# Kernel optimization log

Hardware: AMD Instinct MI355X
Metric: run time of the kernel (lower is better)

Reference implementation:

```python
import jax, jax.numpy as jnp
import numpy as np
from jax import lax


def setup_inputs() -> dict:
    key = jax.random.key(0)
    kx, kw = jax.random.split(key)
    x = jax.random.normal(kx, (32, 3, 8192), dtype=jnp.float32)
    weight = jax.random.normal(kw, (128, 3, 64), dtype=jnp.float32)
    return {"x": x, "weight": weight}


def reference(x, weight):
    # x: [B, C, L], weight: [O, C, K]
    K = weight.shape[2]
    # Cross-correlation (conv1d, no bias, valid padding): [B, O, L-K+1]
    conv_out = lax.conv_general_dilated(
        x, weight, window_strides=(1,), padding='VALID',
        dimension_numbers=('NCH', 'OIH', 'NCH'))
    # Half squared norm of each shapelet: [O]
    w_norm = jnp.sum(weight ** 2, axis=(1, 2)) / 2
    # Half squared norm of each length-K window, via cumulative sums
    # (avoids materializing the [B, C, W, K] unfold tensor)
    sq = jnp.sum(x ** 2, axis=1)               # [B, L]
    c = jnp.pad(jnp.cumsum(sq, axis=1), ((0, 0), (1, 0)))  # [B, L+1]
    win_norm = (c[:, K:] - c[:, :-K]) / 2      # [B, L-K+1]
    # features = conv_out - (||w||^2/2 + ||window||^2/2)
    features = conv_out - w_norm[None, :, None] - win_norm[:, None, :]
    # global max-pool over time, then *(-2) -> min squared distance
    return -2.0 * jnp.max(features, axis=-1)   # [B, O]
```

## Files before the change

### kernel.cpp

```cpp
#include <hip/hip_runtime.h>
#include <float.h>

#define BB 32
#define LL 8192
#define OO 128
#define KK 64
#define WW (LL - KK + 1)
#define NCH 2
#define GX 16

typedef __attribute__((ext_vector_type(8))) short short8;
typedef __attribute__((ext_vector_type(4))) float f32x4;

union AB { int4 i4; int i[4]; short8 v; };

static __device__ __forceinline__ unsigned int f2bf(float f) {
    unsigned int u = __builtin_bit_cast(unsigned int, f);
    return (u + 0x7FFFu + ((u >> 16) & 1u)) >> 16;
}

__global__ __launch_bounds__(256) void prep_kernel(const float* __restrict__ w,
                                                   unsigned short* __restrict__ wswz,
                                                   float* __restrict__ wn) {
    int g = blockIdx.x * 256 + threadIdx.x;
    if (g < 3072) {
        int ob = (g >= 1536) ? 1 : 0;
        int gg = g - ob * 1536;
        int ksqp = gg >> 6;
        int o2   = gg & 63;
        int ks = ksqp >> 2, qp = ksqp & 3;
        int c = ks >> 1, h = ks & 1;
        const float4* p = (const float4*)(w + (ob * 64 + o2) * 192 + c * 64 + h * 32 + qp * 8);
        float4 v0 = p[0], v1 = p[1];
        int4 pk;
        pk.x = (int)(f2bf(v0.x) | (f2bf(v0.y) << 16));
        pk.y = (int)(f2bf(v0.z) | (f2bf(v0.w) << 16));
        pk.z = (int)(f2bf(v1.x) | (f2bf(v1.y) << 16));
        pk.w = (int)(f2bf(v1.z) | (f2bf(v1.w) << 16));
        ((int4*)wswz)[g] = pk;
    }
    int oo = g - 3072;
    if (oo >= 0 && oo < OO) {
        const float* p = w + oo * 192;
        float s = 0.f;
        for (int i = 0; i < 192; ++i) { float v = p[i]; s = fmaf(v, v, s); }
        wn[oo] = 0.5f * s;
    }
}

static __device__ __forceinline__ void stage_chunk(const float* __restrict__ x, int b, int T0,
                                                   unsigned short* xl, float* sql, float* Pl,
                                                   int tid) {
    if (tid < 240) {
        int c = tid / 80, j4 = tid - c * 80;
        int l = T0 + j4 * 4;
        float4 v = make_float4(0.f, 0.f, 0.f, 0.f);
        if (l < LL) v = *(const float4*)(x + (b * 3 + c) * LL + l);
        uint2 pk;
        pk.x = f2bf(v.x) | (f2bf(v.y) << 16);
        pk.y = f2bf(v.z) | (f2bf(v.w) << 16);
        *(uint2*)(xl + c * 320 + j4 * 4) = pk;
    }
    {
        int l = T0 + tid;
        float s = 0.f;
        if (l < LL) {
            #pragma unroll
            for (int c = 0; c < 3; ++c) {
                float v = x[(b * 3 + c) * LL + l];
                s = fmaf(v, v, s);
            }
        }
        sql[tid] = s;
        float s8 = s + __shfl_xor(s, 1, 64);
        s8 += __shfl_xor(s8, 2, 64);
        s8 += __shfl_xor(s8, 4, 64);
        if ((tid & 7) == 0) Pl[tid >> 3] = s8;
    }
    if (tid < 64) {
        int j = 256 + tid, l = T0 + j;
        float s = 0.f;
        if (l < LL) {
            #pragma unroll
            for (int c = 0; c < 3; ++c) {
                float v = x[(b * 3 + c) * LL + l];
                s = fmaf(v, v, s);
            }
        }
        sql[j] = s;
        float s8 = s + __shfl_xor(s, 1, 64);
        s8 += __shfl_xor(s8, 2, 64);
        s8 += __shfl_xor(s8, 4, 64);
        if ((tid & 7) == 0) Pl[32 + (tid >> 3)] = s8;
    }
}

__global__ __launch_bounds__(256, 3) void shapeconv_main(const float* __restrict__ x,
                                                         const unsigned short* __restrict__ wswz,
                                                         const float* __restrict__ wn,
                                                         float* __restrict__ partial) {
    __shared__ __align__(16) unsigned short w_lds[64 * 192];
    __shared__ __align__(16) unsigned short x_lds[2][3 * 320];
    __shared__ __align__(16) float sq_lds[2][320];
    __shared__ float P_lds[2][40];
    __shared__ float mred[64];

    const int tcx = blockIdx.x;
    const int ob = blockIdx.y;
    const int b  = blockIdx.z;
    const int tid = threadIdx.x;
    const int wv = tid >> 6;
    const int lane = tid & 63;
    const int wo = wv & 1, wt = wv >> 1;
    const int n  = lane & 15;
    const int qp = lane >> 4;
    const int Tb = tcx * (NCH * 256);

    {
        const char* src = (const char*)(wswz + ob * 1536 * 8) + tid * 16;
        #pragma unroll
        for (int i = 0; i < 6; ++i) {
            __builtin_amdgcn_global_load_lds(
                (const __attribute__((address_space(1))) unsigned int*)(src + i * 4096),
                (__attribute__((address_space(3))) unsigned int*)((char*)w_lds + wv * 1024 + i * 4096),
                16, 0, 0);
        }
    }

    float wnv[2][4];
    #pragma unroll
    for (int ot = 0; ot < 2; ++ot)
        #pragma unroll
        for (int rg = 0; rg < 4; ++rg)
            wnv[ot][rg] = wn[ob * 64 + 32 * wo + 16 * ot + 4 * qp + rg];

    stage_chunk(x, b, Tb, x_lds[0], sq_lds[0], P_lds[0], tid);

    float m2[2][4];
    #pragma unroll
    for (int ot = 0; ot < 2; ++ot)
        #pragma unroll
        for (int rg = 0; rg < 4; ++rg) m2[ot][rg] = -FLT_MAX;

    #pragma unroll
    for (int ci = 0; ci < NCH; ++ci) {
        const int bsel = ci & 1;
        const int T0 = Tb + ci * 256;
        __syncthreads();

        if (ci + 1 < NCH)
            stage_chunk(x, b, T0 + 256, x_lds[1 - bsel], sq_lds[1 - bsel], P_lds[1 - bsel], tid);

        float wlm[8];
        {
            const float* sql = sq_lds[bsel];
            const float* Pl  = P_lds[bsel];
            int a = 16 * wt + n;
            float4 H0 = *(const float4*)(sql + 8 * a);
            float4 H1 = *(const float4*)(sql + 8 * a + 4);
            float4 G0 = *(const float4*)(sql + 8 * a + 64);
            float4 G1 = *(const float4*)(sql + 8 * a + 68);
            float h[8] = {H0.x, H0.y, H0.z, H0.w, H1.x, H1.y, H1.z, H1.w};
            float g[8] = {G0.x, G0.y, G0.z, G0.w, G1.x, G1.y, G1.z, G1.w};
            float s = 0.f;
            #pragma unroll
            for (int i = 1; i <= 7; ++i) s += Pl[a + i];
            #pragma unroll
            for (int j = 0; j < 8; ++j) s += h[j];
            int tg0 = T0 + 8 * a;
            #pragma unroll
            for (int r = 0; r < 8; ++r) {
                wlm[r] = (tg0 + r < WW) ? 0.5f * s : 1e30f;
                s = s - h[r] + g[r];
            }
        }

        f32x4 acc[2][8];
        #pragma unroll
        for (int ot = 0; ot < 2; ++ot)
            #pragma unroll
            for (int rg = 0; rg < 4; ++rg)
                #pragma unroll
                for (int r = 0; r < 8; ++r)
                    acc[ot][r][rg] = -wnv[ot][rg] - wlm[r];

        const char* xb = (const char*)x_lds[bsel];
        #pragma unroll
        for (int ks = 0; ks < 6; ++ks) {
            int c = ks >> 1, h2 = ks & 1;
            int e0b = c * 640 + 256 * wt + 64 * h2 + 16 * (n + qp);
            int4 Ea = *(const int4*)(xb + e0b);
            int4 Eb = *(const int4*)(xb + e0b + 16);
            int D[8] = {Ea.x, Ea.y, Ea.z, Ea.w, Eb.x, Eb.y, Eb.z, Eb.w};
            AB a0, a1;
            const int4* wq = (const int4*)w_lds + (ks * 4 + qp) * 64 + 32 * wo;
            a0.i4 = wq[n];
            a1.i4 = wq[16 + n];
            #pragma unroll
            for (int r = 0; r < 8; ++r) {
                AB bf;
                int s = r >> 1;
                if ((r & 1) == 0) {
                    bf.i[0] = D[s]; bf.i[1] = D[s + 1]; bf.i[2] = D[s + 2]; bf.i[3] = D[s + 3];
                } else {
                    #pragma unroll
                    for (int d = 0; d < 4; ++d)
                        bf.i[d] = (int)(((unsigned)D[s + d] >> 16) | ((unsigned)D[s + d + 1] << 16));
                }
                acc[0][r] = __builtin_amdgcn_mfma_f32_16x16x32_bf16(a0.v, bf.v, acc[0][r], 0, 0, 0);
                acc[1][r] = __builtin_amdgcn_mfma_f32_16x16x32_bf16(a1.v, bf.v, acc[1][r], 0, 0, 0);
            }
        }

        #pragma unroll
        for (int ot = 0; ot < 2; ++ot)
            #pragma unroll
            for (int rg = 0; rg < 4; ++rg) {
                float mm = m2[ot][rg];
                #pragma unroll
                for (int r = 0; r < 8; ++r) mm = fmaxf(mm, acc[ot][r][rg]);
                m2[ot][rg] = mm;
            }
    }

    #pragma unroll
    for (int s = 1; s <= 8; s <<= 1)
        #pragma unroll
        for (int ot = 0; ot < 2; ++ot)
            #pragma unroll
            for (int rg = 0; rg < 4; ++rg)
                m2[ot][rg] = fmaxf(m2[ot][rg], __shfl_xor(m2[ot][rg], s, 64));

    if (wt == 1 && n == 0) {
        #pragma unroll
        for (int ot = 0; ot < 2; ++ot)
            #pragma unroll
            for (int rg = 0; rg < 4; ++rg)
                mred[32 * wo + 16 * ot + 4 * qp + rg] = m2[ot][rg];
    }
    __syncthreads();
    if (wt == 0 && n == 0) {
        #pragma unroll
        for (int ot = 0; ot < 2; ++ot)
            #pragma unroll
            for (int rg = 0; rg < 4; ++rg) {
                int oi = 32 * wo + 16 * ot + 4 * qp + rg;
                float v = fmaxf(m2[ot][rg], mred[oi]);
                partial[((size_t)(b * GX + tcx) * 2 + ob) * 64 + oi] = v;
            }
    }
}

__global__ __launch_bounds__(256) void reduce_kernel(const float* __restrict__ partial,
                                                     float* __restrict__ out) {
    int idx = blockIdx.x * 256 + threadIdx.x;
    int b = idx >> 7, o = idx & 127;
    const float* pp = partial + ((size_t)b * GX * 2 + (o >> 6)) * 64 + (o & 63);
    float mx = -FLT_MAX;
    #pragma unroll
    for (int t = 0; t < GX; ++t) mx = fmaxf(mx, pp[(size_t)t * 128]);
    out[idx] = -2.f * mx;
}

extern "C" void kernel_launch(void* const* d_in, const int* in_sizes, int n_in,
                              void* d_out, int out_size, void* d_ws, size_t ws_size,
                              hipStream_t stream) {
    const float* x = (const float*)d_in[0];
    const float* w = (const float*)d_in[1];
    float* out = (float*)d_out;

    unsigned short* wswz = (unsigned short*)d_ws;
    float* wn = (float*)((char*)d_ws + 49152);
    float* partial = (float*)((char*)d_ws + 49664);

    prep_kernel<<<13, 256, 0, stream>>>(w, wswz, wn);
    dim3 grid(GX, 2, BB);
    shapeconv_main<<<grid, 256, 0, stream>>>(x, wswz, wn, partial);
    reduce_kernel<<<16, 256, 0, stream>>>(partial, out);
}
```

Before: 75.08 us.

## Fuse weight prep and final reduction into main conv kernel

Drops the separate prep kernel. Each block now converts its 64 shapelets to bf16 directly into LDS and computes their half squared norms in-kernel. Also drops the reduce kernel: each block merges its partial max into the output through an atomic compare-and-swap min loop, after the output is initialised by a memset to a large value. This removes two launches and the workspace round trip. In exchange, every block redoes the weight conversion (2×32×16 times) and adds atomic contention on the output.

```diff
diff --git a/kernel.cpp b/kernel.cpp
--- a/kernel.cpp
+++ b/kernel.cpp
@@ -17,35 +17,6 @@
 static __device__ __forceinline__ unsigned int f2bf(float f) {
     unsigned int u = __builtin_bit_cast(unsigned int, f);
     return (u + 0x7FFFu + ((u >> 16) & 1u)) >> 16;
-}
-
-__global__ __launch_bounds__(256) void prep_kernel(const float* __restrict__ w,
-                                                   unsigned short* __restrict__ wswz,
-                                                   float* __restrict__ wn) {
-    int g = blockIdx.x * 256 + threadIdx.x;
-    if (g < 3072) {
-        int ob = (g >= 1536) ? 1 : 0;
-        int gg = g - ob * 1536;
-        int ksqp = gg >> 6;
-        int o2   = gg & 63;
-        int ks = ksqp >> 2, qp = ksqp & 3;
-        int c = ks >> 1, h = ks & 1;
-        const float4* p = (const float4*)(w + (ob * 64 + o2) * 192 + c * 64 + h * 32 + qp * 8);
-        float4 v0 = p[0], v1 = p[1];
-        int4 pk;
-        pk.x = (int)(f2bf(v0.x) | (f2bf(v0.y) << 16));
-        pk.y = (int)(f2bf(v0.z) | (f2bf(v0.w) << 16));
-        pk.z = (int)(f2bf(v1.x) | (f2bf(v1.y) << 16));
-        pk.w = (int)(f2bf(v1.z) | (f2bf(v1.w) << 16));
-        ((int4*)wswz)[g] = pk;
-    }
-    int oo = g - 3072;
-    if (oo >= 0 && oo < OO) {
-        const float* p = w + oo * 192;
-        float s = 0.f;
-        for (int i = 0; i < 192; ++i) { float v = p[i]; s = fmaf(v, v, s); }
-        wn[oo] = 0.5f * s;
-    }
 }
 
 static __device__ __forceinline__ void stage_chunk(const float* __restrict__ x, int b, int T0,
@@ -95,14 +66,14 @@
     }
 }
 
-__global__ __launch_bounds__(256, 3) void shapeconv_main(const float* __restrict__ x,
-                                                         const unsigned short* __restrict__ wswz,
-                                                         const float* __restrict__ wn,
-                                                         float* __restrict__ partial) {
+__global__ __launch_bounds__(256, 3) void shapeconv_fused(const float* __restrict__ x,
+                                                          const float* __restrict__ w,
+                                                          float* __restrict__ out) {
     __shared__ __align__(16) unsigned short w_lds[64 * 192];
     __shared__ __align__(16) unsigned short x_lds[2][3 * 320];
     __shared__ __align__(16) float sq_lds[2][320];
     __shared__ float P_lds[2][40];
+    __shared__ float wn_lds[64];
     __shared__ float mred[64];
 
     const int tcx = blockIdx.x;
@@ -117,25 +88,31 @@
     const int Tb = tcx * (NCH * 256);
 
     {
-        const char* src = (const char*)(wswz + ob * 1536 * 8) + tid * 16;
-        #pragma unroll
-        for (int i = 0; i < 6; ++i) {
-            __builtin_amdgcn_global_load_lds(
-                (const __attribute__((address_space(1))) unsigned int*)(src + i * 4096),
-                (__attribute__((address_space(3))) unsigned int*)((char*)w_lds + wv * 1024 + i * 4096),
-                16, 0, 0);
-        }
-    }
+        int o = tid >> 2, part = tid & 3;
+        const float4* wp = (const float4*)(w + (ob * 64 + o) * 192) + 12 * part;
+        float s = 0.f;
+        #pragma unroll
+        for (int j = 0; j < 6; ++j) {
+            float4 v0 = wp[2 * j], v1 = wp[2 * j + 1];
+            s = fmaf(v0.x, v0.x, s); s = fmaf(v0.y, v0.y, s);
+            s = fmaf(v0.z, v0.z, s); s = fmaf(v0.w, v0.w, s);
+            s = fmaf(v1.x, v1.x, s); s = fmaf(v1.y, v1.y, s);
+            s = fmaf(v1.z, v1.z, s); s = fmaf(v1.w, v1.w, s);
+            int4 pk;
+            pk.x = (int)(f2bf(v0.x) | (f2bf(v0.y) << 16));
+            pk.y = (int)(f2bf(v0.z) | (f2bf(v0.w) << 16));
+            pk.z = (int)(f2bf(v1.x) | (f2bf(v1.y) << 16));
+            pk.w = (int)(f2bf(v1.z) | (f2bf(v1.w) << 16));
+            ((int4*)w_lds)[(6 * part + j) * 64 + o] = pk;
+        }
+        s += __shfl_xor(s, 1, 64);
+        s += __shfl_xor(s, 2, 64);
+        if (part == 0) wn_lds[o] = 0.5f * s;
+    }
+
+    stage_chunk(x, b, Tb, x_lds[0], sq_lds[0], P_lds[0], tid);
 
     float wnv[2][4];
-    #pragma unroll
-    for (int ot = 0; ot < 2; ++ot)
-        #pragma unroll
-        for (int rg = 0; rg < 4; ++rg)
-            wnv[ot][rg] = wn[ob * 64 + 32 * wo + 16 * ot + 4 * qp + rg];
-
-    stage_chunk(x, b, Tb, x_lds[0], sq_lds[0], P_lds[0], tid);
-
     float m2[2][4];
     #pragma unroll
     for (int ot = 0; ot < 2; ++ot)
@@ -147,6 +124,14 @@
         const int bsel = ci & 1;
         const int T0 = Tb + ci * 256;
         __syncthreads();
+
+        if (ci == 0) {
+            #pragma unroll
+            for (int ot = 0; ot < 2; ++ot)
+                #pragma unroll
+                for (int rg = 0; rg < 4; ++rg)
+                    wnv[ot][rg] = wn_lds[32 * wo + 16 * ot + 4 * qp + rg];
+        }
 
         if (ci + 1 < NCH)
             stage_chunk(x, b, T0 + 256, x_lds[1 - bsel], sq_lds[1 - bsel], P_lds[1 - bsel], tid);
@@ -245,21 +230,16 @@
             #pragma unroll
             for (int rg = 0; rg < 4; ++rg) {
                 int oi = 32 * wo + 16 * ot + 4 * qp + rg;
-                float v = fmaxf(m2[ot][rg], mred[oi]);
-                partial[((size_t)(b * GX + tcx) * 2 + ob) * 64 + oi] = v;
-            }
-    }
-}
-
-__global__ __launch_bounds__(256) void reduce_kernel(const float* __restrict__ partial,
-                                                     float* __restrict__ out) {
-    int idx = blockIdx.x * 256 + threadIdx.x;
-    int b = idx >> 7, o = idx & 127;
-    const float* pp = partial + ((size_t)b * GX * 2 + (o >> 6)) * 64 + (o & 63);
-    float mx = -FLT_MAX;
-    #pragma unroll
-    for (int t = 0; t < GX; ++t) mx = fmaxf(mx, pp[(size_t)t * 128]);
-    out[idx] = -2.f * mx;
+                float v = -2.f * fmaxf(m2[ot][rg], mred[oi]);
+                int* p = (int*)(out + b * OO + ob * 64 + oi);
+                int cur = __hip_atomic_load(p, __ATOMIC_RELAXED, __HIP_MEMORY_SCOPE_AGENT);
+                while (v < __int_as_float(cur)) {
+                    int prev = atomicCAS(p, cur, __float_as_int(v));
+                    if (prev == cur) break;
+                    cur = prev;
+                }
+            }
+    }
 }
 
 extern "C" void kernel_launch(void* const* d_in, const int* in_sizes, int n_in,
@@ -269,12 +249,7 @@
     const float* w = (const float*)d_in[1];
     float* out = (float*)d_out;
 
-    unsigned short* wswz = (unsigned short*)d_ws;
-    float* wn = (float*)((char*)d_ws + 49152);
-    float* partial = (float*)((char*)d_ws + 49664);
-
-    prep_kernel<<<13, 256, 0, stream>>>(w, wswz, wn);
+    hipMemsetAsync(out, 0x7F, (size_t)out_size * sizeof(float), stream);
     dim3 grid(GX, 2, BB);
-    shapeconv_main<<<grid, 256, 0, stream>>>(x, wswz, wn, partial);
-    reduce_kernel<<<16, 256, 0, stream>>>(partial, out);
-}
+    shapeconv_fused<<<grid, 256, 0, stream>>>(x, w, out);
+}
```

Result: slower. 94.42 us (+25.8%).
